# Kernel tuning notes

Hardware: AMD Instinct MI355X
Metric: run time of the kernel (lower is better)

Reference implementation:

```python
import jax, jax.numpy as jnp
import numpy as np

D_MODEL = 1024
N_HEADS = 16
D_HEAD = D_MODEL // N_HEADS


def setup_inputs() -> dict:
    key = jax.random.key(0)
    k_x, k_qkv, k_proj = jax.random.split(key, 3)
    x = jax.random.normal(k_x, (4, 2048, D_MODEL), dtype=jnp.float32)
    # nn.Linear(d_model, 3*d_model, bias=False): weight shape [3*d_model, d_model]
    scale = 1.0 / np.sqrt(D_MODEL)
    W_qkv = jax.random.uniform(k_qkv, (3 * D_MODEL, D_MODEL), dtype=jnp.float32, minval=-scale, maxval=scale)
    W_proj = jax.random.uniform(k_proj, (D_MODEL, D_MODEL), dtype=jnp.float32, minval=-scale, maxval=scale)
    return {"x": x, "W_qkv": W_qkv, "W_proj": W_proj}


def reference(x, W_qkv, W_proj):
    B, T, C = x.shape
    qkv = jnp.einsum('btc,fc->btf', x, W_qkv)  # [B,T,3C]
    q, k, v = jnp.split(qkv, 3, axis=-1)
    # [B,T,H,Dh] -> [B,H,T,Dh]
    q = q.reshape(B, T, N_HEADS, D_HEAD).transpose(0, 2, 1, 3)
    k = k.reshape(B, T, N_HEADS, D_HEAD).transpose(0, 2, 1, 3)
    v = v.reshape(B, T, N_HEADS, D_HEAD).transpose(0, 2, 1, 3)
    att = jnp.einsum('bhqd,bhkd->bhqk', q, k) / jnp.sqrt(jnp.float32(D_HEAD))
    att = jax.nn.softmax(att, axis=-1)
    y = jnp.einsum('bhqk,bhkd->bhqd', att, v)
    y = y.transpose(0, 2, 1, 3).reshape(B, T, C)
    return jnp.einsum('btc,oc->bto', y, W_proj)
```

## Files before the change

### kernel.cpp

```cpp
#include <hip/hip_runtime.h>
#include <stdint.h>
#include <stddef.h>

#define SEQ   2048
#define NH    16
#define DH    64
#define DM    1024
#define NTOK  8192

typedef unsigned short u16;
typedef unsigned int u32;
typedef short bf16x8 __attribute__((ext_vector_type(8)));
typedef float f32x4  __attribute__((ext_vector_type(4)));
typedef unsigned short u16x4 __attribute__((ext_vector_type(4)));
typedef unsigned short u16x8 __attribute__((ext_vector_type(8)));

#define QSCALE 0.18033688011112042f

#define WAIT_VM12 0x0F7C
#define WAIT_VM4  0x0F74
#define WAIT_VM0  0x0F70

__device__ __forceinline__ u16 f2bf(float f) {
  union { float f; unsigned u; } v; v.f = f;
  return (u16)((v.u + 0x7FFFu + ((v.u >> 16) & 1u)) >> 16);
}

__device__ __forceinline__ void gload_lds16(const void* g, void* l) {
  __builtin_amdgcn_global_load_lds(
      (const __attribute__((address_space(1))) void*)g,
      (__attribute__((address_space(3))) void*)l, 16, 0, 0);
}

__global__ __launch_bounds__(256) void cast_kernel(const float* __restrict__ src,
                                                   u16* __restrict__ dst, int n4) {
  int i = blockIdx.x * 256 + threadIdx.x;
  if (i < n4) {
    const float4 f = ((const float4*)src)[i];
    u16x4 o;
    o.x = f2bf(f.x); o.y = f2bf(f.y); o.z = f2bf(f.z); o.w = f2bf(f.w);
    ((u16x4*)dst)[i] = o;
  }
}

__global__ __launch_bounds__(256) void pack_b(const float* __restrict__ W,
                                              u16* __restrict__ Bp, int NS) {
  const int chunk = blockIdx.x * 256 + threadIdx.x;
  const int lane = chunk & 63, blk = chunk >> 6;
  const int c = blk / NS, s = blk % NS;
  const int n = s * 16 + (lane & 15);
  const int k0 = c * 32 + (lane >> 4) * 8;
  const float4 f0 = *(const float4*)&W[(size_t)n * DM + k0];
  const float4 f1 = *(const float4*)&W[(size_t)n * DM + k0 + 4];
  u16x8 o;
  o[0] = f2bf(f0.x); o[1] = f2bf(f0.y); o[2] = f2bf(f0.z); o[3] = f2bf(f0.w);
  o[4] = f2bf(f1.x); o[5] = f2bf(f1.y); o[6] = f2bf(f1.z); o[7] = f2bf(f1.w);
  *(u16x8*)&Bp[(size_t)chunk * 8] = o;
}

template <int EPI>
__global__ __launch_bounds__(256) void gemm_flat(
    const u16* __restrict__ A, const u16* __restrict__ Bp, int NS, int N_,
    u16* __restrict__ Qo, u16* __restrict__ Ko, u16* __restrict__ Vto,
    float* __restrict__ Co) {
  __shared__ __align__(16) u16 sA[2][128 * 64];
  const int tid = threadIdx.x;
  const int wave = tid >> 6, lane = tid & 63;
  const int l16 = lane & 15, quad = lane >> 4;
  const int sw = l16 & 7;
  const int wm = (wave >> 1) * 64, wn = (wave & 1) * 64;
  const int row0 = blockIdx.y * 128, col0 = blockIdx.x * 128;
  const int ck0 = ((quad ^ sw) << 3);
  const int ck1 = (((quad + 4) ^ sw) << 3);
  const int scol = (col0 + wn) >> 4;
  const u16* bpw = Bp + (size_t)lane * 8;

  f32x4 acc[4][4];
  for (int a = 0; a < 4; ++a)
    for (int b = 0; b < 4; ++b) acc[a][b] = (f32x4){0.f, 0.f, 0.f, 0.f};

  bf16x8 bfr[2][2][4];

  for (int j = 0; j < 4; ++j) {
    const int li = j * 256 + tid;
    const int r = li >> 3;
    const int cs = (((li & 7) ^ (r & 7)) << 3);
    gload_lds16(A + (size_t)(row0 + r) * DM + cs, (char*)sA[0] + li * 16);
  }
  for (int kk = 0; kk < 2; ++kk) {
    const u16* bb = bpw + ((size_t)kk * NS + scol) * 512;
    for (int i = 0; i < 4; ++i)
      bfr[0][kk][i] = *(const bf16x8*)(bb + i * 512);
  }

#pragma unroll 2
  for (int t = 0; t < 16; ++t) {
    const int cur = t & 1;
    const int tn = (t + 1) & 15;
    const int k1 = tn << 6;
    for (int j = 0; j < 4; ++j) {
      const int li = j * 256 + tid;
      const int r = li >> 3;
      const int cs = (((li & 7) ^ (r & 7)) << 3);
      gload_lds16(A + (size_t)(row0 + r) * DM + k1 + cs, (char*)sA[cur ^ 1] + li * 16);
    }
    for (int kk = 0; kk < 2; ++kk) {
      const u16* bb = bpw + ((size_t)(tn * 2 + kk) * NS + scol) * 512;
      for (int i = 0; i < 4; ++i)
        bfr[cur ^ 1][kk][i] = *(const bf16x8*)(bb + i * 512);
    }
    __builtin_amdgcn_s_waitcnt(WAIT_VM12);
    __builtin_amdgcn_s_barrier();
    const u16* sa = sA[cur];
    for (int kk = 0; kk < 2; ++kk) {
      const int cko = kk ? ck1 : ck0;
      bf16x8 af[4];
      for (int i = 0; i < 4; ++i)
        af[i] = *(const bf16x8*)&sa[(wm + i * 16 + l16) * 64 + cko];
      for (int mi = 0; mi < 4; ++mi)
        for (int ni = 0; ni < 4; ++ni)
          acc[mi][ni] = __builtin_amdgcn_mfma_f32_16x16x32_bf16(
              af[mi], bfr[cur][kk][ni], acc[mi][ni], 0, 0, 0);
    }
    __builtin_amdgcn_s_barrier();
  }
  __builtin_amdgcn_s_waitcnt(WAIT_VM0);

  if (EPI == 0) {
    const int which = col0 >> 10;
    for (int mi = 0; mi < 4; ++mi)
      for (int ni = 0; ni < 4; ++ni) {
        const int rowb = row0 + wm + mi * 16 + quad * 4;
        const int col = col0 + wn + ni * 16 + l16;
        const int b = rowb >> 11, t = rowb & (SEQ - 1);
        const int c = col & (DM - 1);
        const int h = c >> 6, d = c & 63;
        const size_t bh = (size_t)b * NH + h;
        if (which == 2) {
          u16x4 pk;
          pk.x = f2bf(acc[mi][ni][0]); pk.y = f2bf(acc[mi][ni][1]);
          pk.z = f2bf(acc[mi][ni][2]); pk.w = f2bf(acc[mi][ni][3]);
          *(u16x4*)&Vto[(bh * DH + d) * SEQ + t] = pk;
        } else {
          for (int r = 0; r < 4; ++r) {
            const float v = acc[mi][ni][r];
            if (which == 0) Qo[(bh * SEQ + t + r) * DH + d] = f2bf(v * QSCALE);
            else            Ko[(bh * SEQ + t + r) * DH + d] = f2bf(v);
          }
        }
      }
  } else {
    for (int mi = 0; mi < 4; ++mi)
      for (int ni = 0; ni < 4; ++ni)
        for (int r = 0; r < 4; ++r) {
          const int row = row0 + wm + mi * 16 + quad * 4 + r;
          const int col = col0 + wn + ni * 16 + l16;
          Co[(size_t)row * N_ + col] = acc[mi][ni][r];
        }
  }
}

#define PSTRIDE 72
__global__ __launch_bounds__(256) void flash_attn(
    const u16* __restrict__ Q, const u16* __restrict__ Kk,
    const u16* __restrict__ Vt, u16* __restrict__ Y) {
  __shared__ __align__(16) u16 sK[2][64 * 64];
  __shared__ __align__(16) u16 sV[2][64 * 64];
  __shared__ __align__(16) u16 sP[4 * 64 * PSTRIDE];
  const int tid = threadIdx.x, wave = tid >> 6, lane = tid & 63;
  const int l16 = lane & 15, quad = lane >> 4;
  const int sw = l16 & 7;
  const int ck0 = ((quad ^ sw) << 3);
  const int ck1 = (((quad + 4) ^ sw) << 3);
  const int rloc = tid >> 3;
  const int cs = (((tid & 7) ^ (rloc & 7)) << 3);
  const int bh = blockIdx.y;
  const int q0 = blockIdx.x * 256 + wave * 64;
  const size_t qkBase = (size_t)bh * SEQ * DH;
  const size_t vtBase = (size_t)bh * DH * SEQ;

  bf16x8 qf[4][2];
  for (int ms = 0; ms < 4; ++ms) {
    const u16* qrow = Q + qkBase + (size_t)(q0 + ms * 16 + l16) * DH;
    qf[ms][0] = *(const bf16x8*)(qrow + quad * 8);
    qf[ms][1] = *(const bf16x8*)(qrow + 32 + quad * 8);
  }

  bf16x8 onesf;
  for (int i = 0; i < 8; ++i) onesf[i] = (short)0x3F80;

  f32x4 o[4][4];
  f32x4 osum[4];
  for (int a = 0; a < 4; ++a) {
    osum[a] = (f32x4){0.f, 0.f, 0.f, 0.f};
    for (int b = 0; b < 4; ++b) o[a][b] = (f32x4){0.f, 0.f, 0.f, 0.f};
  }

  u16* myP = sP + wave * 64 * PSTRIDE;

  for (int j = 0; j < 2; ++j) {
    const int r = j * 32 + rloc;
    gload_lds16(Kk + qkBase + (size_t)r * DH + cs, (char*)sK[0] + (j * 256 + tid) * 16);
    gload_lds16(Vt + vtBase + (size_t)r * SEQ + cs, (char*)sV[0] + (j * 256 + tid) * 16);
  }
  for (int t = 0; t < 32; ++t) {
    const int cur = t & 1;
    const int kt1 = ((t + 1) & 31) * 64;
    for (int j = 0; j < 2; ++j) {
      const int r = j * 32 + rloc;
      gload_lds16(Kk + qkBase + (size_t)(kt1 + r) * DH + cs, (char*)sK[cur ^ 1] + (j * 256 + tid) * 16);
      gload_lds16(Vt + vtBase + (size_t)r * SEQ + kt1 + cs, (char*)sV[cur ^ 1] + (j * 256 + tid) * 16);
    }
    __builtin_amdgcn_s_waitcnt(WAIT_VM4);
    __builtin_amdgcn_s_barrier();
    const u16* sk = sK[cur];
    const u16* sv = sV[cur];

    for (int nt = 0; nt < 4; ++nt) {
      bf16x8 kf0 = *(const bf16x8*)&sk[(nt * 16 + l16) * 64 + ck0];
      bf16x8 kf1 = *(const bf16x8*)&sk[(nt * 16 + l16) * 64 + ck1];
      for (int ms = 0; ms < 4; ++ms) {
        f32x4 st = (f32x4){0.f, 0.f, 0.f, 0.f};
        __builtin_amdgcn_s_setprio(1);
        st = __builtin_amdgcn_mfma_f32_16x16x32_bf16(kf0, qf[ms][0], st, 0, 0, 0);
        st = __builtin_amdgcn_mfma_f32_16x16x32_bf16(kf1, qf[ms][1], st, 0, 0, 0);
        __builtin_amdgcn_s_setprio(0);
        const u32 u0 = __builtin_bit_cast(u32, __builtin_amdgcn_exp2f(st[0]));
        const u32 u1 = __builtin_bit_cast(u32, __builtin_amdgcn_exp2f(st[1]));
        const u32 u2 = __builtin_bit_cast(u32, __builtin_amdgcn_exp2f(st[2]));
        const u32 u3 = __builtin_bit_cast(u32, __builtin_amdgcn_exp2f(st[3]));
        uint2 pk;
        pk.x = __builtin_amdgcn_perm(u1, u0, 0x07060302u);
        pk.y = __builtin_amdgcn_perm(u3, u2, 0x07060302u);
        *(uint2*)&myP[(ms * 16 + l16) * PSTRIDE + nt * 16 + quad * 4] = pk;
      }
    }

    bf16x8 pf[4][2];
    for (int ms = 0; ms < 4; ++ms) {
      pf[ms][0] = *(const bf16x8*)&myP[(ms * 16 + l16) * PSTRIDE + quad * 8];
      pf[ms][1] = *(const bf16x8*)&myP[(ms * 16 + l16) * PSTRIDE + 32 + quad * 8];
    }
    __builtin_amdgcn_s_setprio(1);
    for (int ms = 0; ms < 4; ++ms) {
      osum[ms] = __builtin_amdgcn_mfma_f32_16x16x32_bf16(pf[ms][0], onesf, osum[ms], 0, 0, 0);
      osum[ms] = __builtin_amdgcn_mfma_f32_16x16x32_bf16(pf[ms][1], onesf, osum[ms], 0, 0, 0);
    }
    for (int ds = 0; ds < 4; ++ds) {
      bf16x8 vf0 = *(const bf16x8*)&sv[(ds * 16 + l16) * 64 + ck0];
      bf16x8 vf1 = *(const bf16x8*)&sv[(ds * 16 + l16) * 64 + ck1];
      for (int ms = 0; ms < 4; ++ms) {
        o[ms][ds] = __builtin_amdgcn_mfma_f32_16x16x32_bf16(pf[ms][0], vf0, o[ms][ds], 0, 0, 0);
        o[ms][ds] = __builtin_amdgcn_mfma_f32_16x16x32_bf16(pf[ms][1], vf1, o[ms][ds], 0, 0, 0);
      }
    }
    __builtin_amdgcn_s_setprio(0);
    __builtin_amdgcn_s_barrier();
  }
  __builtin_amdgcn_s_waitcnt(WAIT_VM0);

  float rl[4][4];
  for (int ms = 0; ms < 4; ++ms)
    for (int r = 0; r < 4; ++r)
      rl[ms][r] = __frcp_rn(osum[ms][r]);

  const int b = bh >> 4, h = bh & (NH - 1);
  for (int ms = 0; ms < 4; ++ms)
    for (int ds = 0; ds < 4; ++ds)
      for (int r = 0; r < 4; ++r) {
        const int t = q0 + ms * 16 + quad * 4 + r;
        const int d = ds * 16 + l16;
        Y[((size_t)(b * SEQ + t)) * DM + h * DH + d] = f2bf(o[ms][ds][r] * rl[ms][r]);
      }
}

extern "C" void kernel_launch(void* const* d_in, const int* in_sizes, int n_in,
                              void* d_out, int out_size, void* d_ws, size_t ws_size,
                              hipStream_t stream) {
  const float* x     = (const float*)d_in[0];
  const float* Wqkv  = (const float*)d_in[1];
  const float* Wproj = (const float*)d_in[2];
  float* out = (float*)d_out;

  u16* xb     = (u16*)d_ws;
  u16* bpQkv  = xb + (size_t)NTOK * DM;
  u16* bpProj = bpQkv + (size_t)3 * DM * DM;
  u16* Qb  = bpProj + (size_t)DM * DM;
  u16* Kb  = Qb + (size_t)NTOK * DM;
  u16* Vtb = Kb + (size_t)NTOK * DM;
  u16* Yb  = Vtb + (size_t)NTOK * DM;

  {
    int n4 = NTOK * DM / 4;
    cast_kernel<<<(n4 + 255) / 256, 256, 0, stream>>>(x, xb, n4);
    pack_b<<<3 * DM * DM / 8 / 256, 256, 0, stream>>>(Wqkv, bpQkv, 3 * DM / 16);
    pack_b<<<DM * DM / 8 / 256, 256, 0, stream>>>(Wproj, bpProj, DM / 16);
  }

  gemm_flat<0><<<dim3(3 * DM / 128, NTOK / 128), 256, 0, stream>>>(
      xb, bpQkv, 3 * DM / 16, 3 * DM, Qb, Kb, Vtb, nullptr);

  flash_attn<<<dim3(SEQ / 256, 4 * NH), 256, 0, stream>>>(Qb, Kb, Vtb, Yb);

  gemm_flat<1><<<dim3(DM / 128, NTOK / 128), 256, 0, stream>>>(
      Yb, bpProj, DM / 16, DM, nullptr, nullptr, nullptr, out);
}
```

Before: 268.0 us.

## Enlarge GEMM tiles to 256x128 with 512 threads and split MFMA phases with priority

Both projection GEMMs now use 256-row by 128-column tiles with eight waves, so each workgroup reuses the packed B fragments across twice as many rows and the grid has half as many blocks. The inner k-step is split into four MFMA phases separated by barriers and wrapped in s_setprio, with the second A-fragment LDS read placed between phases. The aim is to overlap LDS reads with MFMA work and to cut global B traffic. The cost is 64KB of LDS per block, extra barriers per iteration and fewer blocks per CU, which may hurt occupancy.

```diff
diff --git a/kernel.cpp b/kernel.cpp
--- a/kernel.cpp
+++ b/kernel.cpp
@@ -59,17 +59,17 @@
 }
 
 template <int EPI>
-__global__ __launch_bounds__(256) void gemm_flat(
+__global__ __launch_bounds__(512) void gemm_big(
     const u16* __restrict__ A, const u16* __restrict__ Bp, int NS, int N_,
     u16* __restrict__ Qo, u16* __restrict__ Ko, u16* __restrict__ Vto,
     float* __restrict__ Co) {
-  __shared__ __align__(16) u16 sA[2][128 * 64];
+  __shared__ __align__(16) u16 sA[2][256 * 64];
   const int tid = threadIdx.x;
   const int wave = tid >> 6, lane = tid & 63;
   const int l16 = lane & 15, quad = lane >> 4;
   const int sw = l16 & 7;
   const int wm = (wave >> 1) * 64, wn = (wave & 1) * 64;
-  const int row0 = blockIdx.y * 128, col0 = blockIdx.x * 128;
+  const int row0 = blockIdx.y * 256, col0 = blockIdx.x * 128;
   const int ck0 = ((quad ^ sw) << 3);
   const int ck1 = (((quad + 4) ^ sw) << 3);
   const int scol = (col0 + wn) >> 4;
@@ -82,16 +82,14 @@
   bf16x8 bfr[2][2][4];
 
   for (int j = 0; j < 4; ++j) {
-    const int li = j * 256 + tid;
+    const int li = j * 512 + tid;
     const int r = li >> 3;
     const int cs = (((li & 7) ^ (r & 7)) << 3);
     gload_lds16(A + (size_t)(row0 + r) * DM + cs, (char*)sA[0] + li * 16);
   }
-  for (int kk = 0; kk < 2; ++kk) {
-    const u16* bb = bpw + ((size_t)kk * NS + scol) * 512;
+  for (int kk = 0; kk < 2; ++kk)
     for (int i = 0; i < 4; ++i)
-      bfr[0][kk][i] = *(const bf16x8*)(bb + i * 512);
-  }
+      bfr[0][kk][i] = *(const bf16x8*)(bpw + ((size_t)kk * NS + scol + i) * 512);
 
 #pragma unroll 2
   for (int t = 0; t < 16; ++t) {
@@ -99,29 +97,49 @@
     const int tn = (t + 1) & 15;
     const int k1 = tn << 6;
     for (int j = 0; j < 4; ++j) {
-      const int li = j * 256 + tid;
+      const int li = j * 512 + tid;
       const int r = li >> 3;
       const int cs = (((li & 7) ^ (r & 7)) << 3);
       gload_lds16(A + (size_t)(row0 + r) * DM + k1 + cs, (char*)sA[cur ^ 1] + li * 16);
     }
-    for (int kk = 0; kk < 2; ++kk) {
-      const u16* bb = bpw + ((size_t)(tn * 2 + kk) * NS + scol) * 512;
+    for (int kk = 0; kk < 2; ++kk)
       for (int i = 0; i < 4; ++i)
-        bfr[cur ^ 1][kk][i] = *(const bf16x8*)(bb + i * 512);
-    }
+        bfr[cur ^ 1][kk][i] = *(const bf16x8*)(bpw + ((size_t)(tn * 2 + kk) * NS + scol + i) * 512);
     __builtin_amdgcn_s_waitcnt(WAIT_VM12);
     __builtin_amdgcn_s_barrier();
     const u16* sa = sA[cur];
-    for (int kk = 0; kk < 2; ++kk) {
-      const int cko = kk ? ck1 : ck0;
-      bf16x8 af[4];
-      for (int i = 0; i < 4; ++i)
-        af[i] = *(const bf16x8*)&sa[(wm + i * 16 + l16) * 64 + cko];
+    bf16x8 af0[4], af1[4];
+    for (int mi = 0; mi < 4; ++mi)
+      af0[mi] = *(const bf16x8*)&sa[(wm + mi * 16 + l16) * 64 + ck0];
+    __builtin_amdgcn_s_setprio(1);
+    for (int ni = 0; ni < 2; ++ni)
       for (int mi = 0; mi < 4; ++mi)
-        for (int ni = 0; ni < 4; ++ni)
-          acc[mi][ni] = __builtin_amdgcn_mfma_f32_16x16x32_bf16(
-              af[mi], bfr[cur][kk][ni], acc[mi][ni], 0, 0, 0);
-    }
+        acc[mi][ni] = __builtin_amdgcn_mfma_f32_16x16x32_bf16(
+            af0[mi], bfr[cur][0][ni], acc[mi][ni], 0, 0, 0);
+    __builtin_amdgcn_s_setprio(0);
+    __builtin_amdgcn_s_barrier();
+    for (int mi = 0; mi < 4; ++mi)
+      af1[mi] = *(const bf16x8*)&sa[(wm + mi * 16 + l16) * 64 + ck1];
+    __builtin_amdgcn_s_setprio(1);
+    for (int ni = 2; ni < 4; ++ni)
+      for (int mi = 0; mi < 4; ++mi)
+        acc[mi][ni] = __builtin_amdgcn_mfma_f32_16x16x32_bf16(
+            af0[mi], bfr[cur][0][ni], acc[mi][ni], 0, 0, 0);
+    __builtin_amdgcn_s_setprio(0);
+    __builtin_amdgcn_s_barrier();
+    __builtin_amdgcn_s_setprio(1);
+    for (int ni = 0; ni < 2; ++ni)
+      for (int mi = 0; mi < 4; ++mi)
+        acc[mi][ni] = __builtin_amdgcn_mfma_f32_16x16x32_bf16(
+            af1[mi], bfr[cur][1][ni], acc[mi][ni], 0, 0, 0);
+    __builtin_amdgcn_s_setprio(0);
+    __builtin_amdgcn_s_barrier();
+    __builtin_amdgcn_s_setprio(1);
+    for (int ni = 2; ni < 4; ++ni)
+      for (int mi = 0; mi < 4; ++mi)
+        acc[mi][ni] = __builtin_amdgcn_mfma_f32_16x16x32_bf16(
+            af1[mi], bfr[cur][1][ni], acc[mi][ni], 0, 0, 0);
+    __builtin_amdgcn_s_setprio(0);
     __builtin_amdgcn_s_barrier();
   }
   __builtin_amdgcn_s_waitcnt(WAIT_VM0);
@@ -297,11 +315,11 @@
     pack_b<<<DM * DM / 8 / 256, 256, 0, stream>>>(Wproj, bpProj, DM / 16);
   }
 
-  gemm_flat<0><<<dim3(3 * DM / 128, NTOK / 128), 256, 0, stream>>>(
+  gemm_big<0><<<dim3(3 * DM / 128, NTOK / 256), 512, 0, stream>>>(
       xb, bpQkv, 3 * DM / 16, 3 * DM, Qb, Kb, Vtb, nullptr);
 
   flash_attn<<<dim3(SEQ / 256, 4 * NH), 256, 0, stream>>>(Qb, Kb, Vtb, Yb);
 
-  gemm_flat<1><<<dim3(DM / 128, NTOK / 128), 256, 0, stream>>>(
+  gemm_big<1><<<dim3(DM / 128, NTOK / 256), 512, 0, stream>>>(
       Yb, bpProj, DM / 16, DM, nullptr, nullptr, nullptr, out);
 }
```

New measurement: 283.9 us. 1.06x slower.

## Halve B-fragment register buffer and request three blocks per SM in GEMM

Applied to the files above, without the earlier changes.

The GEMM no longer double-buffers B fragments for the whole k-tile. It keeps one register set per k-half and refills each set right after its MFMAs consume it. Launch bounds now ask for three 256-thread blocks per CU. The aim is to cut VGPR use so more waves stay resident to hide memory latency. The cost is a shorter prefetch distance for B loads, which may expose global-load latency before the next iteration's MFMAs.

```diff
diff --git a/kernel.cpp b/kernel.cpp
--- a/kernel.cpp
+++ b/kernel.cpp
@@ -59,7 +59,7 @@
 }
 
 template <int EPI>
-__global__ __launch_bounds__(256) void gemm_flat(
+__global__ __launch_bounds__(256, 3) void gemm_flat(
     const u16* __restrict__ A, const u16* __restrict__ Bp, int NS, int N_,
     u16* __restrict__ Qo, u16* __restrict__ Ko, u16* __restrict__ Vto,
     float* __restrict__ Co) {
@@ -79,7 +79,7 @@
   for (int a = 0; a < 4; ++a)
     for (int b = 0; b < 4; ++b) acc[a][b] = (f32x4){0.f, 0.f, 0.f, 0.f};
 
-  bf16x8 bfr[2][2][4];
+  bf16x8 bfr[2][4];
 
   for (int j = 0; j < 4; ++j) {
     const int li = j * 256 + tid;
@@ -87,11 +87,9 @@
     const int cs = (((li & 7) ^ (r & 7)) << 3);
     gload_lds16(A + (size_t)(row0 + r) * DM + cs, (char*)sA[0] + li * 16);
   }
-  for (int kk = 0; kk < 2; ++kk) {
-    const u16* bb = bpw + ((size_t)kk * NS + scol) * 512;
-    for (int i = 0; i < 4; ++i)
-      bfr[0][kk][i] = *(const bf16x8*)(bb + i * 512);
-  }
+  for (int kk = 0; kk < 2; ++kk)
+    for (int i = 0; i < 4; ++i)
+      bfr[kk][i] = *(const bf16x8*)(bpw + ((size_t)kk * NS + scol + i) * 512);
 
 #pragma unroll 2
   for (int t = 0; t < 16; ++t) {
@@ -104,24 +102,27 @@
       const int cs = (((li & 7) ^ (r & 7)) << 3);
       gload_lds16(A + (size_t)(row0 + r) * DM + k1 + cs, (char*)sA[cur ^ 1] + li * 16);
     }
-    for (int kk = 0; kk < 2; ++kk) {
-      const u16* bb = bpw + ((size_t)(tn * 2 + kk) * NS + scol) * 512;
-      for (int i = 0; i < 4; ++i)
-        bfr[cur ^ 1][kk][i] = *(const bf16x8*)(bb + i * 512);
-    }
     __builtin_amdgcn_s_waitcnt(WAIT_VM12);
     __builtin_amdgcn_s_barrier();
     const u16* sa = sA[cur];
-    for (int kk = 0; kk < 2; ++kk) {
-      const int cko = kk ? ck1 : ck0;
-      bf16x8 af[4];
-      for (int i = 0; i < 4; ++i)
-        af[i] = *(const bf16x8*)&sa[(wm + i * 16 + l16) * 64 + cko];
-      for (int mi = 0; mi < 4; ++mi)
-        for (int ni = 0; ni < 4; ++ni)
-          acc[mi][ni] = __builtin_amdgcn_mfma_f32_16x16x32_bf16(
-              af[mi], bfr[cur][kk][ni], acc[mi][ni], 0, 0, 0);
-    }
+    bf16x8 af[4];
+    for (int i = 0; i < 4; ++i)
+      af[i] = *(const bf16x8*)&sa[(wm + i * 16 + l16) * 64 + ck0];
+    for (int mi = 0; mi < 4; ++mi)
+      for (int ni = 0; ni < 4; ++ni)
+        acc[mi][ni] = __builtin_amdgcn_mfma_f32_16x16x32_bf16(
+            af[mi], bfr[0][ni], acc[mi][ni], 0, 0, 0);
+    for (int i = 0; i < 4; ++i)
+      bfr[0][i] = *(const bf16x8*)(bpw + ((size_t)(tn * 2 + 0) * NS + scol + i) * 512);
+    bf16x8 ag[4];
+    for (int i = 0; i < 4; ++i)
+      ag[i] = *(const bf16x8*)&sa[(wm + i * 16 + l16) * 64 + ck1];
+    for (int mi = 0; mi < 4; ++mi)
+      for (int ni = 0; ni < 4; ++ni)
+        acc[mi][ni] = __builtin_amdgcn_mfma_f32_16x16x32_bf16(
+            ag[mi], bfr[1][ni], acc[mi][ni], 0, 0, 0);
+    for (int i = 0; i < 4; ++i)
+      bfr[1][i] = *(const bf16x8*)(bpw + ((size_t)(tn * 2 + 1) * NS + scol + i) * 512);
     __builtin_amdgcn_s_barrier();
   }
   __builtin_amdgcn_s_waitcnt(WAIT_VM0);
```

Result: slower. 335.8 us (+25.3%).
